# Performance work log

Measured on AMD Instinct MI355X. Metric: run time of the kernel, lower is better.

The kernel has to match this reference:

```python
import math
import jax, jax.numpy as jnp
import numpy as np

NUM_EXPERTS = 8
TOP_K = 2
CAPACITY_FACTOR = 1.0
B, S, H, I = 4, 2048, 1024, 4096


def setup_inputs() -> dict:
    key = jax.random.key(0)
    k_x, k_rw, k_wi, k_wo = jax.random.split(key, 4)
    x = jax.random.normal(k_x, (B, S, H), dtype=jnp.float32)
    # router: nn.Linear(H, E), xavier_uniform weight, zero-ish bias
    lim = math.sqrt(6.0 / (H + NUM_EXPERTS))
    router_w = jax.random.uniform(k_rw, (NUM_EXPERTS, H), minval=-lim, maxval=lim, dtype=jnp.float32)
    router_b = jnp.zeros((NUM_EXPERTS,), dtype=jnp.float32)
    # expert weights (scaled randn for numerical sanity)
    experts_inter = jax.random.normal(k_wi, (NUM_EXPERTS - 1, H, I), dtype=jnp.float32) / math.sqrt(H)
    experts_out = jax.random.normal(k_wo, (NUM_EXPERTS - 1, I, H), dtype=jnp.float32) / math.sqrt(I)
    return {"x": x, "router_w": router_w, "router_b": router_b,
            "experts_inter": experts_inter, "experts_out": experts_out}


def reference(x, router_w, router_b, experts_inter, experts_out):
    batch, seq, hidden = x.shape
    n_exp = router_w.shape[0]
    n_tok = batch * seq
    cap = math.ceil(n_tok / n_exp * CAPACITY_FACTOR)  # expert capacity

    # router: linear + softmax
    logits = jnp.einsum('bsh,eh->bse', x, router_w) + router_b
    weights_flat = jax.nn.softmax(logits, axis=-1).reshape(n_tok, n_exp)
    x_flat = x.reshape(n_tok, hidden)

    # top-k gating; scatter topk values back into a dense [N, E] matrix
    topk_vals, topk_idx = jax.lax.top_k(weights_flat, TOP_K)
    rows = jnp.arange(n_tok)[:, None]
    topk_flat = jnp.zeros_like(weights_flat).at[rows, topk_idx].set(topk_vals)
    routing_mask = (topk_flat > 0).astype(jnp.int32)

    # no-op path = last expert column (identity * gate weight)
    noop_w = topk_flat[:, -1]
    noop_mask = routing_mask[:, -1].astype(x.dtype)

    # real experts: columns 0..E-2; capacity-limited dispatch via per-column sort
    expert_w = topk_flat[:, :-1]           # [N, E-1]
    expert_mask = routing_mask[:, :-1]     # [N, E-1]
    sorted_indices = jnp.argsort(-expert_mask, axis=0)[:cap]          # [cap, E-1]
    sorted_mask = jnp.take_along_axis(expert_mask, sorted_indices, axis=0)
    used_idx = (sorted_indices * sorted_mask).reshape(-1)             # masked -> index 0

    inputs = x_flat[used_idx] * sorted_mask.reshape(-1).astype(x.dtype)[:, None]
    inputs = inputs.reshape(cap, n_exp - 1, hidden)                   # [cap, E-1, H]
    in_w = jnp.take_along_axis(expert_w, sorted_indices, axis=0)      # [cap, E-1]

    # batched per-expert FFN
    h = jax.nn.relu(jnp.einsum('ceh,ehi->cei', inputs, experts_inter))
    out = jnp.einsum('cei,eih->ceh', h, experts_out) * in_w[..., None]

    # scatter-combine (masked slots write zeros into row 0, harmless)
    combined = jnp.zeros_like(x_flat).at[used_idx].add(out.reshape(-1, hidden))
    combined = combined + x_flat * (noop_w * noop_mask)[:, None]
    return combined.reshape(batch, seq, hidden)
```

## Files before the change

### kernel.cpp

```cpp
#include <hip/hip_runtime.h>
#include <hip/hip_bf16.h>
#include <stdint.h>
#include <stddef.h>


#define N_TOK   8192
#define HDIM    1024
#define IDIM    4096
#define NEXP    7
#define CAP     1024

typedef __bf16 bf16_t;
typedef bf16_t bf16x8 __attribute__((ext_vector_type(8)));
typedef float  f32x4  __attribute__((ext_vector_type(4)));

typedef __attribute__((address_space(3))) char lds_char_t;
typedef __attribute__((address_space(1))) const char glob_char_t;

__device__ __forceinline__ void load_lds16(const void* g, void* l) {
    __builtin_amdgcn_global_load_lds((glob_char_t*)(uintptr_t)g,
                                     (lds_char_t*)(uintptr_t)l, 16, 0, 0);
}

__device__ __forceinline__ bf16x8 pack8(const float* v) {
    bf16x8 r;
#pragma unroll
    for (int j = 0; j < 8; j++) r[j] = (bf16_t)v[j];
    return r;
}

__global__ __launch_bounds__(256) void router_kernel(
    const float* __restrict__ x, const float* __restrict__ rw,
    const float* __restrict__ rb, float* __restrict__ routew,
    float* __restrict__ out)
{
    const int wave = threadIdx.x >> 6, lane = threadIdx.x & 63;
    const int t = blockIdx.x * 4 + wave;
    const float4* xr = (const float4*)(x + (size_t)t * HDIM);
    float4 xv[4];
#pragma unroll
    for (int r = 0; r < 4; r++) xv[r] = xr[lane + r * 64];
    float p[8];
#pragma unroll
    for (int e = 0; e < 8; e++) {
        const float4* wr = (const float4*)(rw + (size_t)e * HDIM);
        float s = 0.f;
#pragma unroll
        for (int r = 0; r < 4; r++) {
            float4 wv = wr[lane + r * 64];
            s += xv[r].x * wv.x + xv[r].y * wv.y + xv[r].z * wv.z + xv[r].w * wv.w;
        }
#pragma unroll
        for (int o = 32; o; o >>= 1) s += __shfl_xor(s, o, 64);
        p[e] = s + rb[e];
    }
    float m = p[0];
#pragma unroll
    for (int e = 1; e < 8; e++) m = fmaxf(m, p[e]);
    float sum = 0.f;
#pragma unroll
    for (int e = 0; e < 8; e++) { p[e] = expf(p[e] - m); sum += p[e]; }
    float inv = 1.f / sum;
#pragma unroll
    for (int e = 0; e < 8; e++) p[e] *= inv;
    int i1 = 0;
#pragma unroll
    for (int e = 1; e < 8; e++) if (p[e] > p[i1]) i1 = e;
    int i2 = (i1 == 0) ? 1 : 0;
#pragma unroll
    for (int e = 0; e < 8; e++) if (e != i1 && p[e] > p[i2]) i2 = e;
    if (lane == 0) {
#pragma unroll
        for (int c = 0; c < 8; c++)
            routew[(size_t)t * 8 + c] = (c == i1) ? p[i1] : ((c == i2) ? p[i2] : 0.f);
    }
    const float c7 = (i1 == 7 || i2 == 7) ? p[7] : 0.f;
    float4* o = (float4*)(out + (size_t)t * HDIM);
#pragma unroll
    for (int r = 0; r < 4; r++) {
        float4 v = xv[r];
        v.x *= c7; v.y *= c7; v.z *= c7; v.w *= c7;
        o[lane + r * 64] = v;
    }
}

__global__ __launch_bounds__(1024) void compact_kernel(
    const float* __restrict__ routew, int* __restrict__ list,
    float* __restrict__ wsel)
{
    const int e = blockIdx.x;
    const int tid = threadIdx.x, wave = tid >> 6, lane = tid & 63;
    for (int i = tid; i < CAP; i += 1024) { list[e * CAP + i] = -1; wsel[e * CAP + i] = 0.f; }
    __shared__ int cnt[16];
    __syncthreads();
    int base = 0;
    const unsigned long long below = (lane == 63) ? ~0ull >> 1 : ((1ull << lane) - 1);
    for (int chunk = 0; chunk < N_TOK / 1024; chunk++) {
        const int t = chunk * 1024 + tid;
        const float w = routew[(size_t)t * 8 + e];
        const bool sel = (w > 0.f);
        const unsigned long long mask = __ballot(sel);
        const int rnk = __popcll(mask & below);
        if (lane == 0) cnt[wave] = __popcll(mask);
        __syncthreads();
        int pre = base;
        for (int w2 = 0; w2 < wave; w2++) pre += cnt[w2];
        const int rank = pre + rnk;
        if (sel && rank < CAP) { list[e * CAP + rank] = t; wsel[e * CAP + rank] = w; }
        int tot = 0;
        for (int w2 = 0; w2 < 16; w2++) tot += cnt[w2];
        base += tot;
        __syncthreads();
    }
}

__global__ __launch_bounds__(128) void gather_kernel(
    const float* __restrict__ x, const int* __restrict__ list,
    bf16_t* __restrict__ A)
{
    const int row = blockIdx.x;
    const int t = list[row];
    const int i = threadIdx.x;
    float4 v0 = {0.f, 0.f, 0.f, 0.f}, v1 = v0;
    if (t >= 0) {
        const float4* xs = (const float4*)(x + (size_t)t * HDIM);
        v0 = xs[i * 2];
        v1 = xs[i * 2 + 1];
    }
    bf16x8 o;
    o[0] = (bf16_t)v0.x; o[1] = (bf16_t)v0.y; o[2] = (bf16_t)v0.z; o[3] = (bf16_t)v0.w;
    o[4] = (bf16_t)v1.x; o[5] = (bf16_t)v1.y; o[6] = (bf16_t)v1.z; o[7] = (bf16_t)v1.w;
    ((bf16x8*)(A + (size_t)row * HDIM))[i] = o;
}

template<int K, int N>
__global__ __launch_bounds__(256) void transpose_cvt(
    const float* __restrict__ W, bf16_t* __restrict__ Wt)
{
    __shared__ float Ts[64][65];
    const int t = threadIdx.x;
    const int e = blockIdx.z;
    const int ktile = blockIdx.y * 64, ntile = blockIdx.x * 64;
    const float* We = W + (size_t)e * K * N;
    const int kr = t >> 4, nc = (t & 15) * 4;
#pragma unroll
    for (int j = 0; j < 4; j++) {
        const float4 v = *(const float4*)(We + (size_t)(ktile + kr + j * 16) * N + ntile + nc);
        Ts[nc + 0][kr + j * 16] = v.x;
        Ts[nc + 1][kr + j * 16] = v.y;
        Ts[nc + 2][kr + j * 16] = v.z;
        Ts[nc + 3][kr + j * 16] = v.w;
    }
    __syncthreads();
    const int n = t >> 2, kc = (t & 3) * 16;
    bf16_t* o = Wt + ((size_t)e * N + ntile + n) * K + ktile + kc;
    bf16x8 p0, p1;
#pragma unroll
    for (int i = 0; i < 8; i++) {
        p0[i] = (bf16_t)Ts[n][kc + i];
        p1[i] = (bf16_t)Ts[n][kc + 8 + i];
    }
    ((bf16x8*)o)[0] = p0;
    ((bf16x8*)o)[1] = p1;
}

template<int KDIM, int NDIM, int KSPLIT, bool IS_G1>
__global__ __launch_bounds__(256, 2) void ffn_gemm_t(
    const bf16_t* __restrict__ Ab, const bf16_t* __restrict__ Bt,
    bf16_t* __restrict__ Hout, const int* __restrict__ list,
    const float* __restrict__ wsel, float* __restrict__ out)
{
    constexpr int BM = 256, BN = 128, BK = 32;
    constexpr int KLEN = KDIM / KSPLIT;
    constexpr int NT = KLEN / BK;
    constexpr int STG = 8192 + 4096;
    __shared__ __align__(16) bf16_t smem[3 * STG];
    const int tid = threadIdx.x, wave = tid >> 6, lane = tid & 63;
    const int e = blockIdx.z / KSPLIT, ks = blockIdx.z % KSPLIT;
    const int mblk = blockIdx.y * BM, nblk = blockIdx.x * BN;

    const bf16_t* Ae = Ab + ((size_t)e * CAP + mblk) * KDIM + (size_t)ks * KLEN;
    const bf16_t* Be = Bt + ((size_t)e * NDIM + nblk) * KDIM + (size_t)ks * KLEN;

    const int r = tid >> 2;
    const int cc = tid & 3;
    const int c = cc ^ ((r >> 1) & 3);
    const bf16_t* agA = Ae + (size_t)r * KDIM + c * 8;
    const bf16_t* agB = Be + (size_t)r * KDIM + c * 8;
    const int wbase = wave * 512;

    auto stage = [&](int koff, int s) {
        bf16_t* Ad = smem + s * STG + wbase;
        bf16_t* Bd = smem + s * STG + 8192 + wbase;
#pragma unroll
        for (int j = 0; j < 4; j++)
            load_lds16(agA + (size_t)(j * 64) * KDIM + koff, Ad + j * 2048);
#pragma unroll
        for (int j = 0; j < 2; j++)
            load_lds16(agB + (size_t)(j * 64) * KDIM + koff, Bd + j * 2048);
    };

    const int wm = (wave & 1) * 128, wn = (wave >> 1) * 64;
    const int lr = lane & 15, q = lane >> 4;
    const int sw = (q ^ ((lr >> 1) & 3)) * 8;

    f32x4 acc[8][4] = {};

    stage(0, 0);
    stage(BK, 1);

    int pb = 0;
    for (int kt = 0; kt < NT; kt++) {
        if (kt + 2 < NT) {
            int nb = pb + 2; if (nb >= 3) nb -= 3;
            stage((kt + 2) * BK, nb);
            asm volatile("s_waitcnt vmcnt(12)" ::: "memory");
        } else if (kt + 2 == NT) {
            asm volatile("s_waitcnt vmcnt(6)" ::: "memory");
        } else {
            asm volatile("s_waitcnt vmcnt(0)" ::: "memory");
        }
        asm volatile("s_barrier" ::: "memory");

        const bf16_t* Ap = smem + pb * STG;
        const bf16_t* Bp = smem + pb * STG + 8192;
        bf16x8 af[8], bfr[4];
#pragma unroll
        for (int i = 0; i < 8; i++)
            af[i] = *(const bf16x8*)(Ap + (wm + i * 16 + lr) * BK + sw);
#pragma unroll
        for (int j = 0; j < 4; j++)
            bfr[j] = *(const bf16x8*)(Bp + (wn + j * 16 + lr) * BK + sw);
#pragma unroll
        for (int i = 0; i < 8; i++)
#pragma unroll
            for (int j = 0; j < 4; j++)
                acc[i][j] = __builtin_amdgcn_mfma_f32_16x16x32_bf16(af[i], bfr[j], acc[i][j], 0, 0, 0);

        if (kt + 1 < NT) {
            asm volatile("s_waitcnt lgkmcnt(0)" ::: "memory");
            asm volatile("s_barrier" ::: "memory");
        }
        pb = (pb == 2) ? 0 : pb + 1;
    }

    if (IS_G1) {
        bf16_t* Ho = Hout + ((size_t)e * CAP + mblk) * NDIM + nblk;
#pragma unroll
        for (int i = 0; i < 8; i++) {
            const int r0 = wm + i * 16 + q * 4;
#pragma unroll
            for (int reg = 0; reg < 4; reg++) {
                bf16_t* row = Ho + (size_t)(r0 + reg) * NDIM;
#pragma unroll
                for (int j = 0; j < 4; j++)
                    row[wn + j * 16 + lr] = (bf16_t)fmaxf(acc[i][j][reg], 0.f);
            }
        }
    } else {
#pragma unroll
        for (int i = 0; i < 8; i++) {
            const int r0 = mblk + wm + i * 16 + q * 4;
#pragma unroll
            for (int reg = 0; reg < 4; reg++) {
                const int row = r0 + reg;
                const int tok = list[e * CAP + row];
                const float wgt = wsel[e * CAP + row];
                if (tok >= 0) {
                    float* orow = out + (size_t)tok * NDIM + nblk;
#pragma unroll
                    for (int j = 0; j < 4; j++)
                        atomicAdd(orow + wn + j * 16 + lr, acc[i][j][reg] * wgt);
                }
            }
        }
    }
}

template<int KDIM, int NDIM, bool IS_G1>
__global__ __launch_bounds__(256) void ffn_gemm_fused(
    const bf16_t* __restrict__ Ab, const float* __restrict__ Wb,
    bf16_t* __restrict__ Hout, const int* __restrict__ list,
    const float* __restrict__ wsel, float* __restrict__ out)
{
    constexpr int BM = 128, BN = 128, BK = 32;
    __shared__ __align__(16) bf16_t As[BM * BK];
    __shared__ __align__(16) bf16_t Bs[BN * BK];
    const int tid = threadIdx.x, wave = tid >> 6, lane = tid & 63;
    const int e = blockIdx.z, mblk = blockIdx.y * BM, nblk = blockIdx.x * BN;

    const bf16_t* Ae = Ab + ((size_t)e * CAP + mblk) * KDIM;
    const float*  We = Wb + (size_t)e * KDIM * NDIM + nblk;

    const int ar = tid >> 2, ac = (tid & 3) * 8;
    const bf16_t* ag0 = Ae + (size_t)ar * KDIM + ac;
    const bf16_t* ag1 = ag0 + (size_t)64 * KDIM;
    bf16_t* as0 = As + wave * 512;
    bf16_t* as1 = As + 2048 + wave * 512;

    const int bn = tid & 127, bc = (tid >> 7) * 2;
    const float* bg = We + bn;
    bf16_t* bsw0 = Bs + bn * BK + ((bc ^ (bn & 3)) * 8);
    bf16_t* bsw1 = Bs + bn * BK + (((bc + 1) ^ (bn & 3)) * 8);

    const int wm = (wave & 1) * 64, wn = (wave >> 1) * 64;
    const int lr = lane & 15, q = lane >> 4;
    const int swz = q ^ ((wn + lr) & 3);

    f32x4 acc[4][4] = {};

    for (int k0 = 0; k0 < KDIM; k0 += BK) {
        load_lds16(ag0 + k0, as0);
        load_lds16(ag1 + k0, as1);
        const float* bp = bg + (size_t)(k0 + bc * 8) * NDIM;
        float v[16];
#pragma unroll
        for (int j = 0; j < 16; j++) v[j] = bp[(size_t)j * NDIM];
        bf16x8 p0 = pack8(v), p1 = pack8(v + 8);
        *(bf16x8*)bsw0 = p0;
        *(bf16x8*)bsw1 = p1;
        __syncthreads();
        bf16x8 af[4], bfr[4];
#pragma unroll
        for (int i = 0; i < 4; i++)
            af[i] = *(const bf16x8*)(As + (wm + i * 16 + lr) * BK + q * 8);
#pragma unroll
        for (int j = 0; j < 4; j++)
            bfr[j] = *(const bf16x8*)(Bs + (wn + j * 16 + lr) * BK + swz * 8);
#pragma unroll
        for (int i = 0; i < 4; i++)
#pragma unroll
            for (int j = 0; j < 4; j++)
                acc[i][j] = __builtin_amdgcn_mfma_f32_16x16x32_bf16(af[i], bfr[j], acc[i][j], 0, 0, 0);
        __syncthreads();
    }

    if (IS_G1) {
        bf16_t* Ho = Hout + ((size_t)e * CAP + mblk) * NDIM + nblk;
#pragma unroll
        for (int i = 0; i < 4; i++) {
            const int r0 = wm + i * 16 + q * 4;
#pragma unroll
            for (int reg = 0; reg < 4; reg++) {
                bf16_t* row = Ho + (size_t)(r0 + reg) * NDIM;
#pragma unroll
                for (int j = 0; j < 4; j++)
                    row[wn + j * 16 + lr] = (bf16_t)fmaxf(acc[i][j][reg], 0.f);
            }
        }
    } else {
#pragma unroll
        for (int i = 0; i < 4; i++) {
            const int r0 = mblk + wm + i * 16 + q * 4;
#pragma unroll
            for (int reg = 0; reg < 4; reg++) {
                const int row = r0 + reg;
                const int tok = list[e * CAP + row];
                const float wgt = wsel[e * CAP + row];
                if (tok >= 0) {
                    float* orow = out + (size_t)tok * NDIM + nblk;
#pragma unroll
                    for (int j = 0; j < 4; j++)
                        atomicAdd(orow + wn + j * 16 + lr, acc[i][j][reg] * wgt);
                }
            }
        }
    }
}

extern "C" void kernel_launch(void* const* d_in, const int* in_sizes, int n_in,
                              void* d_out, int out_size, void* d_ws, size_t ws_size,
                              hipStream_t stream) {
    const float* x  = (const float*)d_in[0];
    const float* rw = (const float*)d_in[1];
    const float* rb = (const float*)d_in[2];
    const float* w1 = (const float*)d_in[3];
    const float* w2 = (const float*)d_in[4];
    float* out = (float*)d_out;

    char* ws = (char*)d_ws;
    float*  routew = (float*)(ws);
    int*    list   = (int*)(ws + 262144);
    float*  wsel   = (float*)(ws + 262144 + 28672);
    bf16_t* Abuf   = (bf16_t*)(ws + 319488);
    bf16_t* Hbuf   = (bf16_t*)(ws + 14999552);
    bf16_t* Wt     = (bf16_t*)(ws + 73719808);

    const size_t NEED = 73719808ull + 58720256ull;

    router_kernel<<<N_TOK / 4, 256, 0, stream>>>(x, rw, rb, routew, out);
    compact_kernel<<<NEXP, 1024, 0, stream>>>(routew, list, wsel);
    gather_kernel<<<NEXP * CAP, 128, 0, stream>>>(x, list, Abuf);

    if (ws_size >= NEED) {
        transpose_cvt<HDIM, IDIM><<<dim3(IDIM / 64, HDIM / 64, NEXP), 256, 0, stream>>>(w1, Wt);
        ffn_gemm_t<HDIM, IDIM, 1, true><<<dim3(IDIM / 128, CAP / 256, NEXP), 256, 0, stream>>>(
            Abuf, Wt, Hbuf, nullptr, nullptr, nullptr);
        transpose_cvt<IDIM, HDIM><<<dim3(HDIM / 64, IDIM / 64, NEXP), 256, 0, stream>>>(w2, Wt);
        ffn_gemm_t<IDIM, HDIM, 4, false><<<dim3(HDIM / 128, CAP / 256, NEXP * 4), 256, 0, stream>>>(
            Hbuf, Wt, nullptr, list, wsel, out);
    } else {
        ffn_gemm_fused<HDIM, IDIM, true><<<dim3(IDIM / 128, CAP / 128, NEXP), 256, 0, stream>>>(
            Abuf, w1, Hbuf, nullptr, nullptr, nullptr);
        ffn_gemm_fused<IDIM, HDIM, false><<<dim3(HDIM / 128, CAP / 128, NEXP), 256, 0, stream>>>(
            Hbuf, w2, nullptr, list, wsel, out);
    }
}
```

Measured before the change: 531.2 us.

## Shrink GEMM tile to 128x128, remap blocks per XCD, reduce split-K

Halves the M tile of the expert FFN GEMMs from 256 to 128 and shrinks the accumulators and LDS stages to match. It replaces the 3D grid with a flat grid whose block index is decoded so that tiles sharing weights or activations land on the same XCD (gid&7), which should improve L2 reuse. The second GEMM's split-K factor drops from 4 to 2, halving the atomic-add traffic to the output. Smaller tiles lower arithmetic intensity per block in exchange for more blocks and better locality, and the launch-bounds occupancy hint is removed.

```diff
diff --git a/kernel.cpp b/kernel.cpp
--- a/kernel.cpp
+++ b/kernel.cpp
@@ -165,19 +165,32 @@
 }
 
 template<int KDIM, int NDIM, int KSPLIT, bool IS_G1>
-__global__ __launch_bounds__(256, 2) void ffn_gemm_t(
+__global__ __launch_bounds__(256) void ffn_gemm_t(
     const bf16_t* __restrict__ Ab, const bf16_t* __restrict__ Bt,
     bf16_t* __restrict__ Hout, const int* __restrict__ list,
     const float* __restrict__ wsel, float* __restrict__ out)
 {
-    constexpr int BM = 256, BN = 128, BK = 32;
+    constexpr int BM = 128, BN = 128, BK = 32;
     constexpr int KLEN = KDIM / KSPLIT;
     constexpr int NT = KLEN / BK;
-    constexpr int STG = 8192 + 4096;
+    constexpr int STG = 4096 + 4096;
     __shared__ __align__(16) bf16_t smem[3 * STG];
     const int tid = threadIdx.x, wave = tid >> 6, lane = tid & 63;
-    const int e = blockIdx.z / KSPLIT, ks = blockIdx.z % KSPLIT;
-    const int mblk = blockIdx.y * BM, nblk = blockIdx.x * BN;
+
+    const int gid = blockIdx.x;
+    const int xcd = gid & 7, t5 = gid >> 3;
+    int e, ks, mt, nt;
+    if (IS_G1) {
+        e  = t5 >> 5; ks = 0;
+        mt = (t5 >> 2) & 7;
+        nt = xcd * 4 + (t5 & 3);
+    } else {
+        const int ez = t5 >> 3, r5 = t5 & 7;
+        e  = ez / KSPLIT; ks = ez % KSPLIT;
+        nt = (xcd & 1) * 4 + (r5 & 3);
+        mt = (xcd >> 1) * 2 + (r5 >> 2);
+    }
+    const int mblk = mt * BM, nblk = nt * BN;
 
     const bf16_t* Ae = Ab + ((size_t)e * CAP + mblk) * KDIM + (size_t)ks * KLEN;
     const bf16_t* Be = Bt + ((size_t)e * NDIM + nblk) * KDIM + (size_t)ks * KLEN;
@@ -191,20 +204,18 @@
 
     auto stage = [&](int koff, int s) {
         bf16_t* Ad = smem + s * STG + wbase;
-        bf16_t* Bd = smem + s * STG + 8192 + wbase;
-#pragma unroll
-        for (int j = 0; j < 4; j++)
-            load_lds16(agA + (size_t)(j * 64) * KDIM + koff, Ad + j * 2048);
-#pragma unroll
-        for (int j = 0; j < 2; j++)
-            load_lds16(agB + (size_t)(j * 64) * KDIM + koff, Bd + j * 2048);
+        bf16_t* Bd = smem + s * STG + 4096 + wbase;
+        load_lds16(agA + koff, Ad);
+        load_lds16(agA + (size_t)64 * KDIM + koff, Ad + 2048);
+        load_lds16(agB + koff, Bd);
+        load_lds16(agB + (size_t)64 * KDIM + koff, Bd + 2048);
     };
 
-    const int wm = (wave & 1) * 128, wn = (wave >> 1) * 64;
+    const int wm = (wave & 1) * 64, wn = (wave >> 1) * 64;
     const int lr = lane & 15, q = lane >> 4;
     const int sw = (q ^ ((lr >> 1) & 3)) * 8;
 
-    f32x4 acc[8][4] = {};
+    f32x4 acc[4][4] = {};
 
     stage(0, 0);
     stage(BK, 1);
@@ -214,25 +225,25 @@
         if (kt + 2 < NT) {
             int nb = pb + 2; if (nb >= 3) nb -= 3;
             stage((kt + 2) * BK, nb);
-            asm volatile("s_waitcnt vmcnt(12)" ::: "memory");
+            asm volatile("s_waitcnt vmcnt(8)" ::: "memory");
         } else if (kt + 2 == NT) {
-            asm volatile("s_waitcnt vmcnt(6)" ::: "memory");
+            asm volatile("s_waitcnt vmcnt(4)" ::: "memory");
         } else {
             asm volatile("s_waitcnt vmcnt(0)" ::: "memory");
         }
         asm volatile("s_barrier" ::: "memory");
 
         const bf16_t* Ap = smem + pb * STG;
-        const bf16_t* Bp = smem + pb * STG + 8192;
-        bf16x8 af[8], bfr[4];
-#pragma unroll
-        for (int i = 0; i < 8; i++)
+        const bf16_t* Bp = smem + pb * STG + 4096;
+        bf16x8 af[4], bfr[4];
+#pragma unroll
+        for (int i = 0; i < 4; i++)
             af[i] = *(const bf16x8*)(Ap + (wm + i * 16 + lr) * BK + sw);
 #pragma unroll
         for (int j = 0; j < 4; j++)
             bfr[j] = *(const bf16x8*)(Bp + (wn + j * 16 + lr) * BK + sw);
 #pragma unroll
-        for (int i = 0; i < 8; i++)
+        for (int i = 0; i < 4; i++)
 #pragma unroll
             for (int j = 0; j < 4; j++)
                 acc[i][j] = __builtin_amdgcn_mfma_f32_16x16x32_bf16(af[i], bfr[j], acc[i][j], 0, 0, 0);
@@ -247,7 +258,7 @@
     if (IS_G1) {
         bf16_t* Ho = Hout + ((size_t)e * CAP + mblk) * NDIM + nblk;
 #pragma unroll
-        for (int i = 0; i < 8; i++) {
+        for (int i = 0; i < 4; i++) {
             const int r0 = wm + i * 16 + q * 4;
 #pragma unroll
             for (int reg = 0; reg < 4; reg++) {
@@ -259,7 +270,7 @@
         }
     } else {
 #pragma unroll
-        for (int i = 0; i < 8; i++) {
+        for (int i = 0; i < 4; i++) {
             const int r0 = mblk + wm + i * 16 + q * 4;
 #pragma unroll
             for (int reg = 0; reg < 4; reg++) {
@@ -394,10 +405,10 @@
 
     if (ws_size >= NEED) {
         transpose_cvt<HDIM, IDIM><<<dim3(IDIM / 64, HDIM / 64, NEXP), 256, 0, stream>>>(w1, Wt);
-        ffn_gemm_t<HDIM, IDIM, 1, true><<<dim3(IDIM / 128, CAP / 256, NEXP), 256, 0, stream>>>(
+        ffn_gemm_t<HDIM, IDIM, 1, true><<<1792, 256, 0, stream>>>(
             Abuf, Wt, Hbuf, nullptr, nullptr, nullptr);
         transpose_cvt<IDIM, HDIM><<<dim3(HDIM / 64, IDIM / 64, NEXP), 256, 0, stream>>>(w2, Wt);
-        ffn_gemm_t<IDIM, HDIM, 4, false><<<dim3(HDIM / 128, CAP / 256, NEXP * 4), 256, 0, stream>>>(
+        ffn_gemm_t<IDIM, HDIM, 2, false><<<896, 256, 0, stream>>>(
             Hbuf, Wt, nullptr, list, wsel, out);
     } else {
         ffn_gemm_fused<HDIM, IDIM, true><<<dim3(IDIM / 128, CAP / 128, NEXP), 256, 0, stream>>>(
```

After: 494.2 us. -7.0%, faster.
